# Kernel optimization log

Measured on AMD Instinct MI355X. Metric: run time of the kernel, lower is better.

Reference implementation:

```python
import jax, jax.numpy as jnp
import numpy as np

N_NODES = 100000
N_EDGES = 1600000
IN_C, HID_C, OUT_C = 32, 64, 32


def setup_inputs() -> dict:
    key = jax.random.key(0)
    ks = jax.random.split(key, 8)
    x = jax.random.normal(ks[0], (N_NODES, IN_C), dtype=jnp.float32)
    edge_index = jax.random.randint(ks[1], (2, N_EDGES), 0, N_NODES, dtype=jnp.int64)
    s = 1.0 / np.sqrt(IN_C)
    W1_l = jax.random.uniform(ks[2], (IN_C, HID_C), jnp.float32, -s, s)
    W1_r = jax.random.uniform(ks[3], (IN_C, HID_C), jnp.float32, -s, s)
    b1 = jnp.zeros((HID_C,), jnp.float32)
    s2 = 1.0 / np.sqrt(HID_C)
    W2_l = jax.random.uniform(ks[4], (HID_C, OUT_C), jnp.float32, -s2, s2)
    W2_r = jax.random.uniform(ks[5], (HID_C, OUT_C), jnp.float32, -s2, s2)
    b2 = jnp.zeros((OUT_C,), jnp.float32)
    return {"x": x, "edge_index": edge_index, "W1_l": W1_l, "b1": b1,
            "W1_r": W1_r, "W2_l": W2_l, "b2": b2, "W2_r": W2_r}


def _sage_conv(x, src, dst, W_l, b_l, W_r):
    # mean-aggregate source features onto destination nodes (PyG SAGEConv)
    n = x.shape[0]
    agg = jax.ops.segment_sum(x[src], dst, num_segments=n)  # [N, C]
    cnt = jax.ops.segment_sum(jnp.ones_like(dst, dtype=x.dtype), dst, num_segments=n)
    agg = agg / jnp.maximum(cnt, 1.0)[:, None]
    return agg @ W_l + b_l + x @ W_r


def reference(x, edge_index, W1_l, b1, W1_r, W2_l, b2, W2_r):
    src, dst = edge_index[0], edge_index[1]
    h = jax.nn.relu(_sage_conv(x, src, dst, W1_l, b1, W1_r))
    # dropout omitted (eval mode, deterministic baseline)
    out = _sage_conv(h, src, dst, W2_l, b2, W2_r)
    return out
```

## Files before the change

### kernel.cpp

```cpp
#include <hip/hip_runtime.h>
#include <hip/hip_bf16.h>
#include <hip/hip_fp16.h>


#define BUCKET_SHIFT 8
#define BUCKET_SPAN  256
#define BUCKET_CAP   8192
#define PART_ITEMS   32
#define PART_TILE    (256 * PART_ITEMS)

__global__ __launch_bounds__(256) void cast_x_kernel(
        const float* __restrict__ x, __half* __restrict__ xh, int total8) {
    int i = blockIdx.x * blockDim.x + threadIdx.x;
    if (i < total8) {
        float4 a = ((const float4*)x)[(size_t)i * 2];
        float4 b = ((const float4*)x)[(size_t)i * 2 + 1];
        struct alignas(16) H8 { __half2 a, b, c, d; } o;
        o.a = __floats2half2_rn(a.x, a.y);
        o.b = __floats2half2_rn(a.z, a.w);
        o.c = __floats2half2_rn(b.x, b.y);
        o.d = __floats2half2_rn(b.z, b.w);
        ((H8*)xh)[i] = o;
    }
}

__global__ __launch_bounds__(256) void partition_kernel(
        const int* __restrict__ src, const int* __restrict__ dst,
        int* __restrict__ cursorB, int* __restrict__ edgesB, int E, int nbuck) {
    __shared__ int hist[512];
    __shared__ int rank_[512];
    __shared__ int base[512];
    const int tid = threadIdx.x;
    const int tbase = blockIdx.x * PART_TILE;

    for (int i = tid; i < 512; i += 256) { hist[i] = 0; rank_[i] = 0; }
    __syncthreads();

#pragma unroll
    for (int it = 0; it < PART_ITEMS; ++it) {
        int idx = tbase + it * 256 + tid;
        if (idx < E) atomicAdd(&hist[dst[idx] >> BUCKET_SHIFT], 1);
    }
    __syncthreads();

    for (int i = tid; i < nbuck; i += 256) {
        int h = hist[i];
        base[i] = h ? atomicAdd(&cursorB[i], h) : 0;
    }
    __syncthreads();

#pragma unroll
    for (int it = 0; it < PART_ITEMS; ++it) {
        int idx = tbase + it * 256 + tid;
        if (idx < E) {
            int d = dst[idx];
            int b = d >> BUCKET_SHIFT;
            int ld = d & (BUCKET_SPAN - 1);
            int r = atomicAdd(&rank_[b], 1);
            edgesB[(size_t)b * BUCKET_CAP + base[b] + r] = (ld << 24) | src[idx];
        }
    }
}

__global__ __launch_bounds__(512) void bucket_scan_kernel(
        const int* __restrict__ cursorB, int* __restrict__ bucketStart, int nbuck) {
    __shared__ int s[512];
    int t = threadIdx.x;
    int v = (t < nbuck) ? cursorB[t] : 0;
    s[t] = v;
    __syncthreads();
    for (int off = 1; off < 512; off <<= 1) {
        int a = (t >= off) ? s[t - off] : 0;
        __syncthreads();
        s[t] += a;
        __syncthreads();
    }
    if (t < nbuck) bucketStart[t] = s[t] - v;
}

__global__ __launch_bounds__(256) void bucket_csr_kernel(
        const int* __restrict__ cursorB, const int* __restrict__ bucketStart,
        const int* __restrict__ edgesB, int* __restrict__ row_start,
        int* __restrict__ sorted_src, int N, int nbuck) {
    __shared__ int cnt[BUCKET_SPAN];
    __shared__ int cur[BUCKET_SPAN];
    __shared__ int sc[BUCKET_SPAN];
    __shared__ int sorted[BUCKET_CAP];

    const int b = blockIdx.x;
    const int t = threadIdx.x;
    const int nodeBase = b << BUCKET_SHIFT;
    const int span = min(BUCKET_SPAN, N - nodeBase);
    const int size = cursorB[b];
    const int gstart = bucketStart[b];
    const int* eb = edgesB + (size_t)b * BUCKET_CAP;

    cnt[t] = 0;
    __syncthreads();
    for (int i = t; i < size; i += 256) atomicAdd(&cnt[((unsigned)eb[i]) >> 24], 1);
    __syncthreads();

    sc[t] = cnt[t];
    __syncthreads();
    for (int off = 1; off < BUCKET_SPAN; off <<= 1) {
        int a = (t >= off) ? sc[t - off] : 0;
        __syncthreads();
        sc[t] += a;
        __syncthreads();
    }
    int excl = sc[t] - cnt[t];
    if (t < span) row_start[nodeBase + t] = gstart + excl;
    if (b == nbuck - 1 && t == 0) row_start[N] = gstart + size;
    cur[t] = excl;
    __syncthreads();

    for (int i = t; i < size; i += 256) {
        int p = eb[i];
        int r = atomicAdd(&cur[((unsigned)p) >> 24], 1);
        sorted[r] = p & 0xFFFFFF;
    }
    __syncthreads();
    for (int i = t; i < size; i += 256) sorted_src[gstart + i] = sorted[i];
}

__device__ __forceinline__ float4 gather_sum_f16(const float2* __restrict__ t2,
                                                 const int* __restrict__ sp,
                                                 int deg, int lane) {
    const int sub = lane & 7;
    const int rowi = lane >> 3;
    float4 acc = make_float4(0.f, 0.f, 0.f, 0.f);
    for (int base = 0; base < deg; base += 64) {
        int chunk = min(deg - base, 64);
        int myidx = (lane < chunk) ? sp[base + lane] : -1;
        int nit = (chunk + 7) >> 3;
        int e[8];
        float2 v[8];
#pragma unroll
        for (int it = 0; it < 8; ++it)
            e[it] = (it < nit) ? __shfl(myidx, it * 8 + rowi) : -1;
#pragma unroll
        for (int it = 0; it < 8; ++it)
            v[it] = (e[it] >= 0) ? t2[(size_t)e[it] * 8 + sub]
                                 : make_float2(0.f, 0.f);
#pragma unroll
        for (int it = 0; it < 8; ++it) {
            const __half2* hp = (const __half2*)&v[it];
            float2 lo = __half22float2(hp[0]);
            float2 hi = __half22float2(hp[1]);
            acc.x += lo.x; acc.y += lo.y; acc.z += hi.x; acc.w += hi.y;
        }
    }
#pragma unroll
    for (int off = 8; off < 64; off <<= 1) {
        acc.x += __shfl_xor(acc.x, off);
        acc.y += __shfl_xor(acc.y, off);
        acc.z += __shfl_xor(acc.z, off);
        acc.w += __shfl_xor(acc.w, off);
    }
    return acc;
}

__global__ __launch_bounds__(512) void layer1_kernel(
        const float* __restrict__ x, const __half* __restrict__ xh,
        const int* __restrict__ row_start, const int* __restrict__ sorted_src,
        const float* __restrict__ W1l, const float* __restrict__ b1,
        const float* __restrict__ W1r, const float* __restrict__ W2l,
        const float* __restrict__ W2r, const float* __restrict__ b2,
        __half* __restrict__ hWh, float* __restrict__ d2, int N) {
    __shared__ float sW1l[32 * 64];
    __shared__ float sW1r[32 * 64];
    __shared__ float sW2l[64 * 32];
    __shared__ float sW2r[64 * 32];
    __shared__ float sb1[64], sb2[32];
    __shared__ float sAgg[8][32], sX[8][32], sH[8][64];

    {
        int t = threadIdx.x;
        ((float4*)sW1l)[t] = ((const float4*)W1l)[t];
        ((float4*)sW1r)[t] = ((const float4*)W1r)[t];
        ((float4*)sW2l)[t] = ((const float4*)W2l)[t];
        ((float4*)sW2r)[t] = ((const float4*)W2r)[t];
        if (t < 64) sb1[t] = b1[t];
        if (t < 32) sb2[t] = b2[t];
    }
    __syncthreads();

    const int w = threadIdx.x >> 6;
    const int lane = threadIdx.x & 63;
    const int n = blockIdx.x * 8 + w;
    if (n >= N) return;

    int rs = row_start[n];
    int re = row_start[n + 1];
    int deg = re - rs;
    float inv = 1.0f / fmaxf((float)deg, 1.0f);
    const float4* x4 = (const float4*)x;

    float4 acc = gather_sum_f16((const float2*)xh, sorted_src + rs, deg, lane);

    if (lane < 8) {
        float4 m;
        m.x = acc.x * inv; m.y = acc.y * inv; m.z = acc.z * inv; m.w = acc.w * inv;
        ((float4*)sAgg[w])[lane] = m;
        ((float4*)sX[w])[lane] = x4[(size_t)n * 8 + lane];
    }

    float accd = sb1[lane];
#pragma unroll
    for (int k = 0; k < 32; ++k)
        accd += sAgg[w][k] * sW1l[k * 64 + lane] + sX[w][k] * sW1r[k * 64 + lane];
    float hv = fmaxf(accd, 0.0f);
    sH[w][lane] = hv;

    const int c2 = lane & 31;
    const int half = lane >> 5;
    float p1 = 0.f, p2 = 0.f;
#pragma unroll
    for (int kk = 0; kk < 32; ++kk) {
        int k = half * 32 + kk;
        float hk = sH[w][k];
        p1 += hk * sW2l[k * 32 + c2];
        p2 += hk * sW2r[k * 32 + c2];
    }
    p1 += __shfl_xor(p1, 32);
    p2 += __shfl_xor(p2, 32);
    if (lane < 32) {
        hWh[(size_t)n * 32 + c2] = __float2half_rn(p1);
        d2[(size_t)n * 32 + c2] = p2 + sb2[c2];
    }
}

__global__ __launch_bounds__(256) void layer2_kernel(
        const __half* __restrict__ hWh, const float* __restrict__ d2,
        const int* __restrict__ row_start, const int* __restrict__ sorted_src,
        float* __restrict__ out, int N) {
    const int w = threadIdx.x >> 6;
    const int lane = threadIdx.x & 63;
    const int n = blockIdx.x * 4 + w;
    if (n >= N) return;

    int rs = row_start[n];
    int re = row_start[n + 1];
    int deg = re - rs;
    float inv = 1.0f / fmaxf((float)deg, 1.0f);

    float4 acc = gather_sum_f16((const float2*)hWh, sorted_src + rs, deg, lane);

    if (lane < 8) {
        float4 dd = ((const float4*)d2)[(size_t)n * 8 + lane];
        float4 o;
        o.x = acc.x * inv + dd.x;
        o.y = acc.y * inv + dd.y;
        o.z = acc.z * inv + dd.z;
        o.w = acc.w * inv + dd.w;
        ((float4*)out)[(size_t)n * 8 + lane] = o;
    }
}

extern "C" void kernel_launch(void* const* d_in, const int* in_sizes, int n_in,
                              void* d_out, int out_size, void* d_ws, size_t ws_size,
                              hipStream_t stream) {
    const float* x   = (const float*)d_in[0];
    const int*   ei  = (const int*)d_in[1];
    const float* W1l = (const float*)d_in[2];
    const float* b1  = (const float*)d_in[3];
    const float* W1r = (const float*)d_in[4];
    const float* W2l = (const float*)d_in[5];
    const float* b2  = (const float*)d_in[6];
    const float* W2r = (const float*)d_in[7];
    float* out = (float*)d_out;

    const int N = in_sizes[0] / 32;
    const int E = in_sizes[1] / 2;
    const int* src = ei;
    const int* dst = ei + E;
    const int NBUCK = (N + BUCKET_SPAN - 1) >> BUCKET_SHIFT;

    char* p = (char*)d_ws;
    auto align64 = [](size_t v) { return (v + 63) & ~(size_t)63; };
    int* cursorB     = (int*)p;    p += align64((size_t)NBUCK * 4);
    int* bucketStart = (int*)p;    p += align64((size_t)(NBUCK + 1) * 4);
    int* row_start   = (int*)p;    p += align64((size_t)(N + 1) * 4);
    int* sorted_src  = (int*)p;    p += align64((size_t)E * 4);
    int* edgesB      = (int*)p;    p += align64((size_t)NBUCK * BUCKET_CAP * 4);
    __half* xh       = (__half*)p; p += align64((size_t)N * 32 * 2);
    __half* hWh      = (__half*)p; p += align64((size_t)N * 32 * 2);
    float* d2        = (float*)p;  p += align64((size_t)N * 32 * 4);

    hipMemsetAsync(cursorB, 0, (size_t)NBUCK * 4, stream);

    int total8 = N * 4;
    cast_x_kernel<<<(total8 + 255) / 256, 256, 0, stream>>>(x, xh, total8);

    int ntiles = (E + PART_TILE - 1) / PART_TILE;
    partition_kernel<<<ntiles, 256, 0, stream>>>(src, dst, cursorB, edgesB, E, NBUCK);
    bucket_scan_kernel<<<1, 512, 0, stream>>>(cursorB, bucketStart, NBUCK);
    bucket_csr_kernel<<<NBUCK, 256, 0, stream>>>(cursorB, bucketStart, edgesB,
                                                 row_start, sorted_src, N, NBUCK);

    layer1_kernel<<<(N + 7) / 8, 512, 0, stream>>>(x, xh, row_start, sorted_src,
                                                   W1l, b1, W1r, W2l, W2r, b2,
                                                   hWh, d2, N);
    layer2_kernel<<<(N + 3) / 4, 256, 0, stream>>>(hWh, d2, row_start, sorted_src,
                                                   out, N);
}
```

Measured before the change: 265.7 us.

## Split layer-1 into gather and fp16 dot2 dense kernel with register weights

Layer 1 is split into a gather kernel that writes the fp16 mean aggregate and a dense kernel that keeps transposed fp16 weights in registers and uses packed fp16 dot2 instructions, handling 4 nodes per wave. A one-block prep kernel transposes and casts the weights. This removes the per-block 32KB shared-memory weight load and the LDS-bound fp32 matvec, which also frees occupancy for the gather. In exchange it adds an extra N×32 fp16 round trip, a weight-prep launch and fp16 rounding of the weights and of x on the self path.

```diff
diff --git a/kernel.cpp b/kernel.cpp
--- a/kernel.cpp
+++ b/kernel.cpp
@@ -8,6 +8,38 @@
 #define BUCKET_CAP   8192
 #define PART_ITEMS   32
 #define PART_TILE    (256 * PART_ITEMS)
+
+typedef _Float16 f16x2 __attribute__((ext_vector_type(2)));
+
+__device__ __forceinline__ float fdot2u(unsigned a, unsigned b, float c) {
+#if __has_builtin(__builtin_amdgcn_fdot2)
+    f16x2 av, bv;
+    __builtin_memcpy(&av, &a, 4);
+    __builtin_memcpy(&bv, &b, 4);
+    return __builtin_amdgcn_fdot2(av, bv, c, false);
+#else
+    __half2 ah = *reinterpret_cast<__half2*>(&a);
+    __half2 bh = *reinterpret_cast<__half2*>(&b);
+    float2 fa = __half22float2(ah), fb = __half22float2(bh);
+    return c + fa.x * fb.x + fa.y * fb.y;
+#endif
+}
+
+__global__ __launch_bounds__(512) void wprep_kernel(
+        const float* __restrict__ W1l, const float* __restrict__ W1r,
+        const float* __restrict__ W2l, const float* __restrict__ W2r,
+        __half* __restrict__ wT) {
+    for (int i = threadIdx.x; i < 8192; i += 512) {
+        int region = i >> 11;
+        int off = i & 2047;
+        float v;
+        if (region == 0)      { int oc = off >> 5, k = off & 31; v = W1l[k * 64 + oc]; }
+        else if (region == 1) { int oc = off >> 5, k = off & 31; v = W1r[k * 64 + oc]; }
+        else if (region == 2) { int c = off >> 6, k = off & 63;  v = W2l[k * 32 + c]; }
+        else                  { int c = off >> 6, k = off & 63;  v = W2r[k * 32 + c]; }
+        wT[i] = __float2half_rn(v);
+    }
+}
 
 __global__ __launch_bounds__(256) void cast_x_kernel(
         const float* __restrict__ x, __half* __restrict__ xh, int total8) {
@@ -160,73 +192,102 @@
     return acc;
 }
 
-__global__ __launch_bounds__(512) void layer1_kernel(
-        const float* __restrict__ x, const __half* __restrict__ xh,
-        const int* __restrict__ row_start, const int* __restrict__ sorted_src,
-        const float* __restrict__ W1l, const float* __restrict__ b1,
-        const float* __restrict__ W1r, const float* __restrict__ W2l,
-        const float* __restrict__ W2r, const float* __restrict__ b2,
-        __half* __restrict__ hWh, float* __restrict__ d2, int N) {
-    __shared__ float sW1l[32 * 64];
-    __shared__ float sW1r[32 * 64];
-    __shared__ float sW2l[64 * 32];
-    __shared__ float sW2r[64 * 32];
-    __shared__ float sb1[64], sb2[32];
-    __shared__ float sAgg[8][32], sX[8][32], sH[8][64];
-
-    {
-        int t = threadIdx.x;
-        ((float4*)sW1l)[t] = ((const float4*)W1l)[t];
-        ((float4*)sW1r)[t] = ((const float4*)W1r)[t];
-        ((float4*)sW2l)[t] = ((const float4*)W2l)[t];
-        ((float4*)sW2r)[t] = ((const float4*)W2r)[t];
-        if (t < 64) sb1[t] = b1[t];
-        if (t < 32) sb2[t] = b2[t];
-    }
-    __syncthreads();
-
+__global__ __launch_bounds__(256) void gather1_kernel(
+        const __half* __restrict__ xh, const int* __restrict__ row_start,
+        const int* __restrict__ sorted_src, __half* __restrict__ aggMh, int N) {
     const int w = threadIdx.x >> 6;
     const int lane = threadIdx.x & 63;
-    const int n = blockIdx.x * 8 + w;
+    const int n = blockIdx.x * 4 + w;
     if (n >= N) return;
 
     int rs = row_start[n];
     int re = row_start[n + 1];
     int deg = re - rs;
     float inv = 1.0f / fmaxf((float)deg, 1.0f);
-    const float4* x4 = (const float4*)x;
 
     float4 acc = gather_sum_f16((const float2*)xh, sorted_src + rs, deg, lane);
 
     if (lane < 8) {
-        float4 m;
-        m.x = acc.x * inv; m.y = acc.y * inv; m.z = acc.z * inv; m.w = acc.w * inv;
-        ((float4*)sAgg[w])[lane] = m;
-        ((float4*)sX[w])[lane] = x4[(size_t)n * 8 + lane];
-    }
-
-    float accd = sb1[lane];
-#pragma unroll
-    for (int k = 0; k < 32; ++k)
-        accd += sAgg[w][k] * sW1l[k * 64 + lane] + sX[w][k] * sW1r[k * 64 + lane];
-    float hv = fmaxf(accd, 0.0f);
-    sH[w][lane] = hv;
-
+        __half2 h0 = __floats2half2_rn(acc.x * inv, acc.y * inv);
+        __half2 h1 = __floats2half2_rn(acc.z * inv, acc.w * inv);
+        unsigned u0, u1;
+        __builtin_memcpy(&u0, &h0, 4);
+        __builtin_memcpy(&u1, &h1, 4);
+        ((uint2*)(aggMh + (size_t)n * 32))[lane] = make_uint2(u0, u1);
+    }
+}
+
+__global__ __launch_bounds__(512) void dense_kernel(
+        const __half* __restrict__ xh, const __half* __restrict__ aggMh,
+        const __half* __restrict__ wT,
+        const float* __restrict__ b1, const float* __restrict__ b2,
+        __half* __restrict__ hWh, float* __restrict__ d2, int N) {
+    __shared__ __align__(16) __half sH[8][64];
+
+    const int w = threadIdx.x >> 6;
+    const int lane = threadIdx.x & 63;
+    const int oc = lane;
     const int c2 = lane & 31;
-    const int half = lane >> 5;
-    float p1 = 0.f, p2 = 0.f;
-#pragma unroll
-    for (int kk = 0; kk < 32; ++kk) {
-        int k = half * 32 + kk;
-        float hk = sH[w][k];
-        p1 += hk * sW2l[k * 32 + c2];
-        p2 += hk * sW2r[k * 32 + c2];
-    }
-    p1 += __shfl_xor(p1, 32);
-    p2 += __shfl_xor(p2, 32);
-    if (lane < 32) {
-        hWh[(size_t)n * 32 + c2] = __float2half_rn(p1);
-        d2[(size_t)n * 32 + c2] = p2 + sb2[c2];
+    const int khalf = lane >> 5;
+
+    const unsigned* wT32 = (const unsigned*)wT;
+    unsigned w1l[16], w1r[16], w2l[16], w2r[16];
+    {
+        const uint4* p1l = (const uint4*)(wT32 + oc * 16);
+        const uint4* p1r = (const uint4*)(wT32 + 1024 + oc * 16);
+        const uint4* p2l = (const uint4*)(wT32 + 2048 + c2 * 32 + khalf * 16);
+        const uint4* p2r = (const uint4*)(wT32 + 3072 + c2 * 32 + khalf * 16);
+#pragma unroll
+        for (int i = 0; i < 4; ++i) {
+            ((uint4*)w1l)[i] = p1l[i];
+            ((uint4*)w1r)[i] = p1r[i];
+            ((uint4*)w2l)[i] = p2l[i];
+            ((uint4*)w2r)[i] = p2r[i];
+        }
+    }
+    const float bias1 = b1[oc];
+    const float bias2 = b2[c2];
+
+#pragma unroll
+    for (int i = 0; i < 4; ++i) {
+        int n = blockIdx.x * 32 + w * 4 + i;
+        if (n >= N) break;
+
+        unsigned ag[16], xr[16];
+        const uint4* pa = (const uint4*)((const unsigned*)aggMh + (size_t)n * 16);
+        const uint4* px = (const uint4*)((const unsigned*)xh + (size_t)n * 16);
+#pragma unroll
+        for (int j = 0; j < 4; ++j) {
+            ((uint4*)ag)[j] = pa[j];
+            ((uint4*)xr)[j] = px[j];
+        }
+
+        float acc = bias1;
+#pragma unroll
+        for (int k = 0; k < 16; ++k) {
+            acc = fdot2u(ag[k], w1l[k], acc);
+            acc = fdot2u(xr[k], w1r[k], acc);
+        }
+        float hv = fmaxf(acc, 0.0f);
+        sH[w][oc] = __float2half_rn(hv);
+
+        unsigned hr[16];
+        const uint4* ph = (const uint4*)((const unsigned*)(&sH[w][0]) + khalf * 16);
+#pragma unroll
+        for (int j = 0; j < 4; ++j) ((uint4*)hr)[j] = ph[j];
+
+        float p1 = 0.f, p2v = 0.f;
+#pragma unroll
+        for (int k = 0; k < 16; ++k) {
+            p1  = fdot2u(hr[k], w2l[k], p1);
+            p2v = fdot2u(hr[k], w2r[k], p2v);
+        }
+        p1  += __shfl_xor(p1, 32);
+        p2v += __shfl_xor(p2v, 32);
+        if (lane < 32) {
+            hWh[(size_t)n * 32 + c2] = __float2half_rn(p1);
+            d2[(size_t)n * 32 + c2] = p2v + bias2;
+        }
     }
 }
 
@@ -284,10 +345,14 @@
     int* sorted_src  = (int*)p;    p += align64((size_t)E * 4);
     int* edgesB      = (int*)p;    p += align64((size_t)NBUCK * BUCKET_CAP * 4);
     __half* xh       = (__half*)p; p += align64((size_t)N * 32 * 2);
+    __half* aggMh    = (__half*)p; p += align64((size_t)N * 32 * 2);
     __half* hWh      = (__half*)p; p += align64((size_t)N * 32 * 2);
     float* d2        = (float*)p;  p += align64((size_t)N * 32 * 4);
+    __half* wT       = (__half*)p; p += align64((size_t)8192 * 2);
 
     hipMemsetAsync(cursorB, 0, (size_t)NBUCK * 4, stream);
+
+    wprep_kernel<<<1, 512, 0, stream>>>(W1l, W1r, W2l, W2r, wT);
 
     int total8 = N * 4;
     cast_x_kernel<<<(total8 + 255) / 256, 256, 0, stream>>>(x, xh, total8);
@@ -298,9 +363,10 @@
     bucket_csr_kernel<<<NBUCK, 256, 0, stream>>>(cursorB, bucketStart, edgesB,
                                                  row_start, sorted_src, N, NBUCK);
 
-    layer1_kernel<<<(N + 7) / 8, 512, 0, stream>>>(x, xh, row_start, sorted_src,
-                                                   W1l, b1, W1r, W2l, W2r, b2,
-                                                   hWh, d2, N);
+    gather1_kernel<<<(N + 3) / 4, 256, 0, stream>>>(xh, row_start, sorted_src,
+                                                    aggMh, N);
+    dense_kernel<<<(N + 31) / 32, 512, 0, stream>>>(xh, aggMh, wT, b1, b2,
+                                                    hWh, d2, N);
     layer2_kernel<<<(N + 3) / 4, 256, 0, stream>>>(hWh, d2, row_start, sorted_src,
                                                    out, N);
 }
```

Result: slower. 272.3 us (+2.5%).
